# Optimization experiments

Measured on AMD Instinct MI355X. Metric: run time of the kernel, lower is better.

Reference implementation:

```python
import jax, jax.numpy as jnp
import numpy as np

NUM_EMBEDDINGS = 4096
EMBED_DIM = 128
COMMITMENT_COST = 0.25
N = 32768


def setup_inputs() -> dict:
    key = jax.random.key(0)
    kx, kw = jax.random.split(key)
    x = jax.random.normal(kx, (N, EMBED_DIM), dtype=jnp.float32)
    # nn.Embedding init: uniform(-1/K, 1/K)
    lim = 1.0 / NUM_EMBEDDINGS
    W = jax.random.uniform(kw, (NUM_EMBEDDINGS, EMBED_DIM), dtype=jnp.float32,
                           minval=-lim, maxval=lim)
    return {"x": x, "W": W}


def reference(x, W):
    distances = (jnp.sum(x * x, axis=1, keepdims=True)
                 + jnp.sum(W * W, axis=1)
                 - 2.0 * jnp.matmul(x, W.T))
    encoding_indices = jnp.argmin(distances, axis=1)            # [N]
    quantized = W[encoding_indices]                              # [N, D] (one-hot matmul == gather)

    sg = jax.lax.stop_gradient
    e_latent_loss = jnp.mean((sg(quantized) - x) ** 2)
    q_latent_loss = jnp.mean((quantized - sg(x)) ** 2)
    loss = q_latent_loss + COMMITMENT_COST * e_latent_loss

    quantized_st = x + sg(quantized - x)                         # straight-through
    quantized_2d = quantized_st[:, :, None, None]                # [N, D, 1, 1]
    return quantized_2d, quantized_st, loss, encoding_indices
```

## Files before the change

### kernel.cpp

```cpp
#include <hip/hip_runtime.h>
#include <hip/hip_bf16.h>

#define NEMB  4096
#define DIM   128
#define NROWS 32768
#define MARGIN 3.5e-4f
#define RPB   128
#define CHUNK 128
#define NITER 32

typedef _Float16 half8  __attribute__((ext_vector_type(8)));
typedef _Float16 half4v __attribute__((ext_vector_type(4)));
typedef _Float16 half2v __attribute__((ext_vector_type(2)));
typedef float    float16v __attribute__((ext_vector_type(16)));

typedef const __attribute__((address_space(1))) void* gas_ptr;
typedef __attribute__((address_space(3))) void*       las_ptr;

__device__ __forceinline__ void gload16(const void* g, void* l) {
    __builtin_amdgcn_global_load_lds((gas_ptr)g, (las_ptr)l, 16, 0, 0);
}

__device__ __forceinline__ half2v hmin2(half2v a, half2v b) {
    half2v r;
    r.x = (a.x < b.x) ? a.x : b.x;
    r.y = (a.y < b.y) ? a.y : b.y;
    return r;
}

__launch_bounds__(256)
__global__ void k_prep(const float* __restrict__ W, _Float16* __restrict__ Wh2,
                       float* __restrict__ sww, _Float16* __restrict__ swwh,
                       double* __restrict__ dsum, int* __restrict__ cnt) {
    const int b = blockIdx.x;
    const int t = threadIdx.x;
    const int rbase = b * 8;

    if (b == 0 && t == 0) { *dsum = 0.0; *cnt = 0; }

    const int i4 = rbase * 32 + t;
    const float4 v = ((const float4*)W)[i4];
    const int r  = i4 >> 5;
    const int k0 = (i4 & 31) * 4;
    const int s  = r >> 5, cs = r & 31, c = k0 >> 4, h2 = (k0 >> 3) & 1, j0 = k0 & 7;
    half4v hv = { (_Float16)(v.x * 65536.0f), (_Float16)(v.y * 65536.0f),
                  (_Float16)(v.z * 65536.0f), (_Float16)(v.w * 65536.0f) };
    *(half4v*)(Wh2 + (s * 8 + c) * 512 + (h2 * 32 + cs) * 8 + j0) = hv;

    if (t < 64) {
        const int row = rbase + (t >> 3);
        const int j   = t & 7;
        const float* p = W + (size_t)row * DIM + j;
        float vv = p[0];
        float rr = __fmul_rn(vv, vv);
        #pragma unroll
        for (int q = 1; q < 16; ++q) { vv = p[q * 8]; rr = __fadd_rn(rr, __fmul_rn(vv, vv)); }
        float o = __shfl_xor(rr, 1, 64); rr = __fadd_rn(rr, o);
        o = __shfl_xor(rr, 2, 64); rr = __fadd_rn(rr, o);
        o = __shfl_xor(rr, 4, 64); rr = __fadd_rn(rr, o);
        if (j == 0) {
            sww[row]  = rr;
            swwh[row] = (_Float16)(rr * 32768.0f);
        }
    }
}

__global__ __launch_bounds__(1024, 4)
void k_main(const float* __restrict__ x, const _Float16* __restrict__ Wh2,
            const float* __restrict__ W, const float* __restrict__ sww,
            const _Float16* __restrict__ swwh,
            float* __restrict__ out0, float* __restrict__ out1,
            float* __restrict__ out_idx, double* __restrict__ dsum,
            int* __restrict__ cnt, float* __restrict__ out_loss) {
    __shared__ __align__(16) _Float16 sA[2 * CHUNK * DIM];
    __shared__ _Float16 gbuf[RPB * 256];
    __shared__ float ssw[NEMB];
    __shared__ _Float16 swwh_lds[NEMB];
    __shared__ float red16[16];

    const int tid  = threadIdx.x;
    const int wv   = tid >> 6;
    const int lane = tid & 63;
    const int l31  = lane & 31;
    const int h    = lane >> 5;
    const int r0   = blockIdx.x * RPB;
    const int mt   = wv & 3;
    const int np   = wv >> 2;

    const int start = (blockIdx.x >> 3) & 31;
    {
        const char* src = (const char*)Wh2 + (size_t)start * (CHUNK * DIM * 2);
        #pragma unroll
        for (int r = 0; r < 2; ++r)
            gload16(src + wv * 2048 + r * 1024 + lane * 16, (char*)sA + wv * 2048 + r * 1024);
    }

    ((float4*)ssw)[tid] = ((const float4*)sww)[tid];
    if (tid < 512) ((float4*)swwh_lds)[tid] = ((const float4*)swwh)[tid];

    half8 bfr[8];
    {
        const float* xr = x + (size_t)(r0 + np * 32 + l31) * DIM + h * 8;
        #pragma unroll
        for (int c = 0; c < 8; ++c) {
            const float4 u0 = *(const float4*)(xr + c * 16);
            const float4 u1 = *(const float4*)(xr + c * 16 + 4);
            bfr[c] = (half8){ (_Float16)u0.x, (_Float16)u0.y, (_Float16)u0.z, (_Float16)u0.w,
                              (_Float16)u1.x, (_Float16)u1.y, (_Float16)u1.z, (_Float16)u1.w };
        }
    }

    half8 bx2 = (_Float16)0.0f;
    if (h == 0) bx2[0] = (_Float16)-1.0f;

    float16v zero16;
    #pragma unroll
    for (int i = 0; i < 16; ++i) zero16[i] = 0.f;

    half8 ax = (_Float16)0.0f;

    float sxx_reg;
    {
        const float* ps = x + (size_t)(r0 + wv * 8 + (lane >> 3)) * DIM + (lane & 7);
        float vv = ps[0];
        float rr = __fmul_rn(vv, vv);
        #pragma unroll
        for (int q = 1; q < 16; ++q) { vv = ps[q * 8]; rr = __fadd_rn(rr, __fmul_rn(vv, vv)); }
        float o = __shfl_xor(rr, 1, 64); rr = __fadd_rn(rr, o);
        o = __shfl_xor(rr, 2, 64); rr = __fadd_rn(rr, o);
        o = __shfl_xor(rr, 4, 64); rr = __fadd_rn(rr, o);
        sxx_reg = rr;
    }

    for (int it = 0; it < NITER; ++it) {
        __syncthreads();
        if (it + 1 < NITER) {
            const int nc = (start + it + 1) & (NITER - 1);
            const char* src = (const char*)Wh2 + (size_t)nc * (CHUNK * DIM * 2);
            char* dst = (char*)sA + ((it + 1) & 1) * (CHUNK * DIM * 2);
            #pragma unroll
            for (int r = 0; r < 2; ++r)
                gload16(src + wv * 2048 + r * 1024 + lane * 16, dst + wv * 2048 + r * 1024);
        }
        const int cb = (start + it) & (NITER - 1);
        const int s  = cb * 4 + mt;

        ax[0] = (h == 0) ? swwh_lds[s * 32 + l31] : (_Float16)0.0f;

        const _Float16* curb = sA + (it & 1) * (CHUNK * DIM);

        float16v acc;
        {
            const half8 a0 = *(const half8*)(curb + (mt * 8 + 0) * 512 + lane * 8);
            acc = __builtin_amdgcn_mfma_f32_32x32x16_f16(a0, bfr[0], zero16, 0, 0, 0);
        }
        #pragma unroll
        for (int c = 1; c < 8; ++c) {
            const half8 a = *(const half8*)(curb + (mt * 8 + c) * 512 + lane * 8);
            acc = __builtin_amdgcn_mfma_f32_32x32x16_f16(a, bfr[c], acc, 0, 0, 0);
        }
        acc = __builtin_amdgcn_mfma_f32_32x32x16_f16(ax, bx2, acc, 0, 0, 0);

        const float mx0 = fmaxf(fmaxf(fmaxf(acc[0], acc[1]), fmaxf(acc[2], acc[3])),
                                fmaxf(fmaxf(acc[4], acc[5]), fmaxf(acc[6], acc[7])));
        const float mx1 = fmaxf(fmaxf(fmaxf(acc[8], acc[9]), fmaxf(acc[10], acc[11])),
                                fmaxf(fmaxf(acc[12], acc[13]), fmaxf(acc[14], acc[15])));
        const float g0 = mx0 * -0x1p-15f;
        const float g1 = mx1 * -0x1p-15f;
        union { half2v h2; int u; } cu, ot;
        cu.h2.x = (_Float16)g0; cu.h2.y = (_Float16)g1;
        ot.u = __shfl_xor(cu.u, 32, 64);
        cu.h2 = hmin2(cu.h2, ot.h2);
        if (h == 0) {
            const int row = np * 32 + l31;
            const int ws  = (s + row) & 127;
            ((int*)gbuf)[row * 128 + ws] = cu.u;
        }
    }

    __syncthreads();

    {
        float4* sAf4 = (float4*)sA;
        const float4* xg4 = (const float4*)(x + (size_t)r0 * DIM);
        #pragma unroll
        for (int i = 0; i < 4; ++i) sAf4[tid + i * 1024] = xg4[tid + i * 1024];
    }
    __syncthreads();
    const float* sAf = (const float*)sA;

    const int cig = lane >> 2;
    const int kp  = lane & 3;
    float p_acc = 0.f;
    for (int t = 0; t < 8; ++t) {
        const int lr  = wv * 8 + t;
        const int row = r0 + lr;

        const int2 gw = *(const int2*)((const char*)gbuf + lr * 512 + lane * 8);
        union { half2v h2; int u; } pa, pb;
        pa.u = gw.x; pb.u = gw.y;
        const float v0 = (float)pa.h2.x, v1 = (float)pa.h2.y;
        const float v2 = (float)pb.h2.x, v3 = (float)pb.h2.y;
        float m = fminf(fminf(v0, v1), fminf(v2, v3));
        #pragma unroll
        for (int off = 1; off < 64; off <<= 1) m = fminf(m, __shfl_xor(m, off, 64));
        const float thr = m + MARGIN;
        unsigned long long bal[4];
        bal[0] = __ballot(v0 <= thr);
        bal[1] = __ballot(v1 <= thr);
        bal[2] = __ballot(v2 <= thr);
        bal[3] = __ballot(v3 <= thr);

        const float sxr = __shfl(sxx_reg, t * 8, 64);
        const float* xl = sAf + lr * DIM;

        float4 xv[8];
        {
            const float4* xq4 = (const float4*)(xl + kp * 32);
            #pragma unroll
            for (int j2 = 0; j2 < 8; ++j2) xv[j2] = xq4[j2];
        }

        float bv = 3.0e38f;
        int   bi = 0x7fffffff;

        #pragma unroll
        for (int j = 0; j < 4; ++j) {
            unsigned long long msk = bal[j];
            while (msk) {
                const int l = __builtin_ctzll(msk);
                msk &= msk - 1;
                const int wsl = 2 * l + (j >> 1);
                const int g   = 2 * ((wsl - lr) & 127) + (j & 1);
                const int c   = g * 16 + cig;
                const float4* wq4 = (const float4*)(W + (size_t)c * DIM + kp * 32);
                float dot = 0.f;
                #pragma unroll
                for (int j2 = 0; j2 < 8; ++j2) {
                    const float4 wv4 = wq4[j2];
                    dot = fmaf(xv[j2].x, wv4.x, dot);
                    dot = fmaf(xv[j2].y, wv4.y, dot);
                    dot = fmaf(xv[j2].z, wv4.z, dot);
                    dot = fmaf(xv[j2].w, wv4.w, dot);
                }
                float o = __shfl_xor(dot, 1, 64); dot = __fadd_rn(dot, o);
                o = __shfl_xor(dot, 2, 64); dot = __fadd_rn(dot, o);
                const float A = __fadd_rn(sxr, ssw[c]);
                const float d = __fsub_rn(A, __fmul_rn(2.0f, dot));
                if (d < bv || (d == bv && c < bi)) { bv = d; bi = c; }
            }
        }
        #pragma unroll
        for (int off = 1; off < 64; off <<= 1) {
            const float ov = __shfl_xor(bv, off, 64);
            const int   oi = __shfl_xor(bi, off, 64);
            if (ov < bv || (ov == bv && oi < bi)) { bv = ov; bi = oi; }
        }

        const float2 wv2 = *(const float2*)(W + (size_t)bi * DIM + lane * 2);
        const float2 xv2 = *(const float2*)(xl + lane * 2);
        const float d0 = wv2.x - xv2.x, d1 = wv2.y - xv2.y;
        const float p = fmaf(d0, d0, d1 * d1);
        *(float2*)(out0 + (size_t)row * DIM + lane * 2) = wv2;
        *(float2*)(out1 + (size_t)row * DIM + lane * 2) = wv2;
        p_acc = __fadd_rn(p_acc, p);
        if (lane == 0) out_idx[row] = (float)bi;
    }
    #pragma unroll
    for (int off = 32; off > 0; off >>= 1) p_acc += __shfl_down(p_acc, off, 64);
    if (lane == 0) red16[wv] = p_acc;
    __syncthreads();
    if (tid < 16) {
        float sblk = red16[tid];
        sblk += __shfl_xor(sblk, 1, 64);
        sblk += __shfl_xor(sblk, 2, 64);
        sblk += __shfl_xor(sblk, 4, 64);
        sblk += __shfl_xor(sblk, 8, 64);
        if (tid == 0) {
            atomicAdd(dsum, (double)sblk);
            __threadfence();
            const int prev = atomicAdd(cnt, 1);
            if (prev == (int)gridDim.x - 1) {
                __threadfence();
                const double tot = atomicAdd(dsum, 0.0);
                out_loss[0] = (float)(tot * (1.25 / ((double)NROWS * (double)DIM)));
            }
        }
    }
}

extern "C" void kernel_launch(void* const* d_in, const int* in_sizes, int n_in,
                              void* d_out, int out_size, void* d_ws, size_t ws_size,
                              hipStream_t stream) {
    const float* x = (const float*)d_in[0];
    const float* W = (const float*)d_in[1];
    float* out = (float*)d_out;

    float* out_q2d  = out;
    float* out_qst  = out + (size_t)NROWS * DIM;
    float* out_loss = out + (size_t)2 * NROWS * DIM;
    float* out_idx  = out + (size_t)2 * NROWS * DIM + 1;

    float* ws   = (float*)d_ws;
    float* sww  = ws;
    double* dsum = (double*)(ws + 4096);
    int*    cnt  = (int*)(ws + 4098);
    _Float16* swwh = (_Float16*)(ws + 8192);
    _Float16* Wh2  = (_Float16*)(ws + 4096 + 32768);

    k_prep<<<NEMB / 8, 256, 0, stream>>>(W, Wh2, sww, swwh, dsum, cnt);
    k_main<<<NROWS / RPB, 1024, 0, stream>>>(x, Wh2, W, sww, swwh,
                                             out_q2d, out_qst, out_idx,
                                             dsum, cnt, out_loss);
}
```

Before: 171.9 us.

## Fuse codebook prep into main kernel with grid-wide atomic barrier

Removes the separate prep kernel launch. Each of the 256 main blocks now converts 16 codebook rows to scaled fp16, computes their norms, and signals completion through an atomic counter. All blocks spin until every block has finished before loading the fp16 codebook. The prep step also writes a permuted fp32 copy of W, so the exact-refine dot products read coalesced float4s per lane instead of strided rows. The spin barrier assumes all 256 blocks are co-resident, otherwise it deadlocks, and it adds a memset plus some global atomics.

Measured after the change: 155.2 us. 9.8% less time.

```diff
diff --git a/kernel.cpp b/kernel.cpp
--- a/kernel.cpp
+++ b/kernel.cpp
@@ -8,6 +8,7 @@
 #define RPB   128
 #define CHUNK 128
 #define NITER 32
+#define NBLK  (NROWS / RPB)
 
 typedef _Float16 half8  __attribute__((ext_vector_type(8)));
 typedef _Float16 half4v __attribute__((ext_vector_type(4)));
@@ -28,50 +29,14 @@
     return r;
 }
 
-__launch_bounds__(256)
-__global__ void k_prep(const float* __restrict__ W, _Float16* __restrict__ Wh2,
-                       float* __restrict__ sww, _Float16* __restrict__ swwh,
-                       double* __restrict__ dsum, int* __restrict__ cnt) {
-    const int b = blockIdx.x;
-    const int t = threadIdx.x;
-    const int rbase = b * 8;
-
-    if (b == 0 && t == 0) { *dsum = 0.0; *cnt = 0; }
-
-    const int i4 = rbase * 32 + t;
-    const float4 v = ((const float4*)W)[i4];
-    const int r  = i4 >> 5;
-    const int k0 = (i4 & 31) * 4;
-    const int s  = r >> 5, cs = r & 31, c = k0 >> 4, h2 = (k0 >> 3) & 1, j0 = k0 & 7;
-    half4v hv = { (_Float16)(v.x * 65536.0f), (_Float16)(v.y * 65536.0f),
-                  (_Float16)(v.z * 65536.0f), (_Float16)(v.w * 65536.0f) };
-    *(half4v*)(Wh2 + (s * 8 + c) * 512 + (h2 * 32 + cs) * 8 + j0) = hv;
-
-    if (t < 64) {
-        const int row = rbase + (t >> 3);
-        const int j   = t & 7;
-        const float* p = W + (size_t)row * DIM + j;
-        float vv = p[0];
-        float rr = __fmul_rn(vv, vv);
-        #pragma unroll
-        for (int q = 1; q < 16; ++q) { vv = p[q * 8]; rr = __fadd_rn(rr, __fmul_rn(vv, vv)); }
-        float o = __shfl_xor(rr, 1, 64); rr = __fadd_rn(rr, o);
-        o = __shfl_xor(rr, 2, 64); rr = __fadd_rn(rr, o);
-        o = __shfl_xor(rr, 4, 64); rr = __fadd_rn(rr, o);
-        if (j == 0) {
-            sww[row]  = rr;
-            swwh[row] = (_Float16)(rr * 32768.0f);
-        }
-    }
-}
-
 __global__ __launch_bounds__(1024, 4)
-void k_main(const float* __restrict__ x, const _Float16* __restrict__ Wh2,
-            const float* __restrict__ W, const float* __restrict__ sww,
-            const _Float16* __restrict__ swwh,
+void k_main(const float* __restrict__ x, const float* __restrict__ W,
+            _Float16* __restrict__ Wh2, float* __restrict__ sww,
+            _Float16* __restrict__ swwh, float* __restrict__ Wp,
             float* __restrict__ out0, float* __restrict__ out1,
             float* __restrict__ out_idx, double* __restrict__ dsum,
-            int* __restrict__ cnt, float* __restrict__ out_loss) {
+            int* __restrict__ cnt, int* __restrict__ done_cnt,
+            float* __restrict__ out_loss) {
     __shared__ __align__(16) _Float16 sA[2 * CHUNK * DIM];
     __shared__ _Float16 gbuf[RPB * 256];
     __shared__ float ssw[NEMB];
@@ -87,16 +52,43 @@
     const int mt   = wv & 3;
     const int np   = wv >> 2;
 
-    const int start = (blockIdx.x >> 3) & 31;
-    {
-        const char* src = (const char*)Wh2 + (size_t)start * (CHUNK * DIM * 2);
-        #pragma unroll
-        for (int r = 0; r < 2; ++r)
-            gload16(src + wv * 2048 + r * 1024 + lane * 16, (char*)sA + wv * 2048 + r * 1024);
-    }
-
-    ((float4*)ssw)[tid] = ((const float4*)sww)[tid];
-    if (tid < 512) ((float4*)swwh_lds)[tid] = ((const float4*)swwh)[tid];
+    {
+        const int rbase = blockIdx.x * 16;
+        if (tid < 512) {
+            const int i4 = rbase * 32 + tid;
+            const float4 v = ((const float4*)W)[i4];
+            const int r  = i4 >> 5;
+            const int m  = i4 & 31;
+            const int k0 = m * 4;
+            const int s  = r >> 5, cs = r & 31, c = k0 >> 4, h2 = (k0 >> 3) & 1, j0 = k0 & 7;
+            half4v hv = { (_Float16)(v.x * 65536.0f), (_Float16)(v.y * 65536.0f),
+                          (_Float16)(v.z * 65536.0f), (_Float16)(v.w * 65536.0f) };
+            *(half4v*)(Wh2 + (s * 8 + c) * 512 + (h2 * 32 + cs) * 8 + j0) = hv;
+            ((float4*)Wp)[(r >> 4) * 512 + (m & 7) * 64 + (r & 15) * 4 + (m >> 3)] = v;
+        }
+        if (tid < 128) {
+            const int row = rbase + (tid >> 3);
+            const int j   = tid & 7;
+            const float* p = W + (size_t)row * DIM + j;
+            float vv = p[0];
+            float rr = __fmul_rn(vv, vv);
+            #pragma unroll
+            for (int q = 1; q < 16; ++q) { vv = p[q * 8]; rr = __fadd_rn(rr, __fmul_rn(vv, vv)); }
+            float o = __shfl_xor(rr, 1, 64); rr = __fadd_rn(rr, o);
+            o = __shfl_xor(rr, 2, 64); rr = __fadd_rn(rr, o);
+            o = __shfl_xor(rr, 4, 64); rr = __fadd_rn(rr, o);
+            if (j == 0) {
+                sww[row]  = rr;
+                swwh[row] = (_Float16)(rr * 32768.0f);
+            }
+        }
+        __syncthreads();
+        if (tid == 0) {
+            __threadfence();
+            __hip_atomic_fetch_add(done_cnt, 1, __ATOMIC_RELEASE,
+                                   __HIP_MEMORY_SCOPE_AGENT);
+        }
+    }
 
     half8 bfr[8];
     {
@@ -131,6 +123,23 @@
         o = __shfl_xor(rr, 4, 64); rr = __fadd_rn(rr, o);
         sxx_reg = rr;
     }
+
+    if (tid == 0) {
+        while (__hip_atomic_load(done_cnt, __ATOMIC_ACQUIRE,
+                                 __HIP_MEMORY_SCOPE_AGENT) < NBLK) { }
+    }
+    __syncthreads();
+
+    const int start = (blockIdx.x >> 3) & 31;
+    {
+        const char* src = (const char*)Wh2 + (size_t)start * (CHUNK * DIM * 2);
+        #pragma unroll
+        for (int r = 0; r < 2; ++r)
+            gload16(src + wv * 2048 + r * 1024 + lane * 16, (char*)sA + wv * 2048 + r * 1024);
+    }
+
+    ((float4*)ssw)[tid] = ((const float4*)sww)[tid];
+    if (tid < 512) ((float4*)swwh_lds)[tid] = ((const float4*)swwh)[tid];
 
     for (int it = 0; it < NITER; ++it) {
         __syncthreads();
@@ -191,6 +200,7 @@
 
     const int cig = lane >> 2;
     const int kp  = lane & 3;
+    const float4* Wp4 = (const float4*)Wp;
     float p_acc = 0.f;
     for (int t = 0; t < 8; ++t) {
         const int lr  = wv * 8 + t;
@@ -233,11 +243,11 @@
                 const int wsl = 2 * l + (j >> 1);
                 const int g   = 2 * ((wsl - lr) & 127) + (j & 1);
                 const int c   = g * 16 + cig;
-                const float4* wq4 = (const float4*)(W + (size_t)c * DIM + kp * 32);
+                const float4* wq4 = Wp4 + g * 512 + lane;
                 float dot = 0.f;
                 #pragma unroll
                 for (int j2 = 0; j2 < 8; ++j2) {
-                    const float4 wv4 = wq4[j2];
+                    const float4 wv4 = wq4[j2 * 64];
                     dot = fmaf(xv[j2].x, wv4.x, dot);
                     dot = fmaf(xv[j2].y, wv4.y, dot);
                     dot = fmaf(xv[j2].z, wv4.z, dot);
@@ -305,11 +315,14 @@
     float* sww  = ws;
     double* dsum = (double*)(ws + 4096);
     int*    cnt  = (int*)(ws + 4098);
+    int*    done = (int*)(ws + 4099);
     _Float16* swwh = (_Float16*)(ws + 8192);
     _Float16* Wh2  = (_Float16*)(ws + 4096 + 32768);
-
-    k_prep<<<NEMB / 8, 256, 0, stream>>>(W, Wh2, sww, swwh, dsum, cnt);
-    k_main<<<NROWS / RPB, 1024, 0, stream>>>(x, Wh2, W, sww, swwh,
-                                             out_q2d, out_qst, out_idx,
-                                             dsum, cnt, out_loss);
+    float*    Wp   = ws + 299008;
+
+    hipMemsetAsync(ws + 4096, 0, 16, stream);
+
+    k_main<<<NBLK, 1024, 0, stream>>>(x, W, Wh2, sww, swwh, Wp,
+                                      out_q2d, out_qst, out_idx,
+                                      dsum, cnt, done, out_loss);
 }
```
